# Performance work log

Hardware: AMD Instinct MI355X
Metric: run time of the kernel (lower is better)

The kernel has to match this reference:

```python
import jax, jax.numpy as jnp
import numpy as np

D = 512      # node_feature_size
LAT = 768    # latent_size
B = 16       # number of graphs
S = 256      # conditioning sequence length
H = 8        # attention heads


def _ln(x, g, b):
    m = x.mean(-1, keepdims=True)
    v = jnp.var(x, axis=-1, keepdims=True)
    return (x - m) / jnp.sqrt(v + 1e-5) * g + b


def setup_inputs() -> dict:
    key = jax.random.key(0)
    ks = jax.random.split(key, 10)
    lengths = np.array([512 + 32 * i for i in range(B)])  # ragged node counts
    N = int(lengths.sum())                                # 12032
    Lmax = int(lengths.max())                             # 992
    graph_batch = jnp.asarray(np.repeat(np.arange(B), lengths), dtype=jnp.int32)
    valid = np.array([S - 8 * i for i in range(B)])
    # torch key_padding_mask semantics: True = position is ignored (padding)
    conditioning_mask = jnp.asarray(np.arange(S)[None, :] >= valid[:, None])
    p = lambda k, sh: jax.random.normal(k, sh, jnp.float32) * 0.02
    return dict(
        graph_nodes=jax.random.normal(ks[0], (N, D), jnp.float32),
        graph_batch=graph_batch,
        conditioning_vector=jax.random.normal(ks[1], (B, S, LAT), jnp.float32),
        conditioning_mask=conditioning_mask,
        max_nodes=Lmax,
        num_heads=H,
        Wq=p(ks[2], (D, D)), bq=jnp.zeros(D, jnp.float32),
        Wk=p(ks[3], (LAT, D)), bk=jnp.zeros(D, jnp.float32),
        Wv=p(ks[4], (LAT, D)), bv=jnp.zeros(D, jnp.float32),
        in_w=p(ks[5], (3, D, D)), in_b=jnp.zeros((3, D), jnp.float32),
        Wo=p(ks[6], (D, D)), bo=jnp.zeros(D, jnp.float32),
        ln1_g=jnp.ones(D, jnp.float32), ln1_b=jnp.zeros(D, jnp.float32),
        W1=p(ks[7], (D, D)), b1=jnp.zeros(D, jnp.float32),
        ln2_g=jnp.ones(D, jnp.float32), ln2_b=jnp.zeros(D, jnp.float32),
    )


def reference(graph_nodes, graph_batch, conditioning_vector, conditioning_mask,
              max_nodes, num_heads, Wq, bq, Wk, bk, Wv, bv, in_w, in_b,
              Wo, bo, ln1_g, ln1_b, W1, b1, ln2_g, ln2_b):
    N, Dm = graph_nodes.shape
    Bn, Sk, _ = conditioning_vector.shape
    dh = Dm // num_heads
    # --- pad ragged node sets to dense [B, Lmax, D] (vectorized scatter) ---
    counts = jax.ops.segment_sum(jnp.ones(N, jnp.int32), graph_batch, num_segments=Bn)
    starts = jnp.concatenate([jnp.zeros(1, jnp.int32), jnp.cumsum(counts)[:-1].astype(jnp.int32)])
    pos = jnp.arange(N, dtype=jnp.int32) - starts[graph_batch]
    dense = jnp.zeros((Bn, max_nodes, Dm), graph_nodes.dtype).at[graph_batch, pos].set(graph_nodes)
    # --- projections ---
    q = dense @ Wq + bq
    k = conditioning_vector @ Wk + bk
    v = conditioning_vector @ Wv + bv
    # --- MultiheadAttention internal in-projections ---
    qh = (q @ in_w[0] + in_b[0]).reshape(Bn, max_nodes, num_heads, dh)
    kh = (k @ in_w[1] + in_b[1]).reshape(Bn, Sk, num_heads, dh)
    vh = (v @ in_w[2] + in_b[2]).reshape(Bn, Sk, num_heads, dh)
    scores = jnp.einsum('blhd,bshd->bhls', qh, kh) / jnp.sqrt(jnp.asarray(dh, qh.dtype))
    scores = jnp.where(conditioning_mask[:, None, None, :], -jnp.inf, scores)
    attn = jax.nn.softmax(scores, axis=-1)     # [B,H,L,S]
    av_attn = attn.mean(axis=1)                # head-averaged weights [B,L,S]
    ctx = jnp.einsum('bhls,bshd->blhd', attn, vh).reshape(Bn, max_nodes, Dm)
    attn_out = ctx @ Wo + bo
    # --- residual + LN + FFN + LN (dropout inactive / eval mode) ---
    x = _ln(attn_out + dense, ln1_g, ln1_b)
    x = jax.nn.leaky_relu(x @ W1 + b1) + x     # slope 0.01 matches nn.LeakyReLU
    x = _ln(x, ln2_g, ln2_b)
    # --- unpad back to ragged [N, D] (vectorized gather) ---
    node_out = x[graph_batch, pos]
    return node_out, av_attn
```

## Files before the change

### kernel.cpp

```cpp
#include <hip/hip_runtime.h>
#include <math.h>

#define D_   512
#define LAT_ 768
#define B_   16
#define S_   256
#define H_   8
#define DH_  64

typedef __bf16 bf16x8 __attribute__((ext_vector_type(8)));
typedef float f32x4 __attribute__((ext_vector_type(4)));

__device__ __forceinline__ unsigned short f2bf(float f) {
  unsigned u = __float_as_uint(f);
  unsigned r = (u + 0x7fffu + ((u >> 16) & 1u)) >> 16;
  return (unsigned short)r;
}

__global__ void prep_k(const void* __restrict__ mask, int* __restrict__ maskc,
                       const int* __restrict__ gb, int* __restrict__ starts, int n) {
  int i = blockIdx.x * blockDim.x + threadIdx.x;
  if (i < B_ * S_) {
    const unsigned char* pb = (const unsigned char*)mask;
    const int*   pi = (const int*)mask;
    const float* pf = (const float*)mask;
    unsigned int w = ((const unsigned int*)mask)[1023];
    int v;
    if (w == 0x01010101u)      v = pb[i];
    else if (w == 0x3f800000u) v = (pf[i] != 0.0f);
    else                       v = (pi[i] != 0);
    maskc[i] = v ? 1 : 0;
  }
  if (i < n) {
    if (i == 0 || gb[i] != gb[i - 1]) starts[gb[i]] = i;
  }
}

__global__ __launch_bounds__(256) void scatter_k(const float* __restrict__ nodes,
    const int* __restrict__ gb, const int* __restrict__ starts,
    float* __restrict__ dense, int Lmax) {
  int i = blockIdx.x;
  int b = gb[i], p = i - starts[b];
  const float* src = nodes + (size_t)i * D_;
  float* dst = dense + ((size_t)b * Lmax + p) * D_;
  dst[threadIdx.x]       = src[threadIdx.x];
  dst[threadIdx.x + 256] = src[threadIdx.x + 256];
}

__device__ __forceinline__ void pack_chunk(const float* __restrict__ W,
    unsigned short* __restrict__ out, int K, int ntoff, int idx) {
  int n = idx & 511, kc = idx >> 9;
  int kt = kc >> 2, kblk = kc & 3;
  int nt = n >> 7, nblk = (n >> 4) & 7, col = n & 15;
  int KT = K >> 5;
  size_t ob = ((size_t)((nt + ntoff) * KT + kt) * 4096) + nblk * 512 + kblk * 128 + col * 8;
  unsigned short v[8];
#pragma unroll
  for (int j = 0; j < 8; ++j) v[j] = f2bf(W[(size_t)(kc * 8 + j) * 512 + n]);
  int4 pk;
  pk.x = v[0] | (v[1] << 16); pk.y = v[2] | (v[3] << 16);
  pk.z = v[4] | (v[5] << 16); pk.w = v[6] | (v[7] << 16);
  *(int4*)&out[ob] = pk;
}

__global__ __launch_bounds__(256) void pack1_k(const float* __restrict__ in_w,
    const float* __restrict__ Wo, const float* __restrict__ W1,
    unsigned short* iw0, unsigned short* iw1, unsigned short* iw2,
    unsigned short* Wo_pk, unsigned short* W1_pk) {
  int bid = blockIdx.x, sel = bid >> 7, within = bid & 127;
  const float* W; unsigned short* out;
  switch (sel) {
    case 0: W = in_w;               out = iw0;   break;
    case 1: W = in_w + 512 * 512;   out = iw1;   break;
    case 2: W = in_w + 2 * 512 * 512; out = iw2; break;
    case 3: W = Wo;                 out = Wo_pk; break;
    default: W = W1;                out = W1_pk; break;
  }
  pack_chunk(W, out, 512, 0, within * 256 + threadIdx.x);
}

__global__ __launch_bounds__(256) void pack2_k(const float* __restrict__ Wqp,
    const float* __restrict__ Wkp, const float* __restrict__ Wvp,
    unsigned short* Wqp_pk, unsigned short* kv_pk) {
  int bid = blockIdx.x, tid = threadIdx.x;
  if (bid < 128)      pack_chunk(Wqp, Wqp_pk, 512, 0, bid * 256 + tid);
  else if (bid < 320) pack_chunk(Wkp, kv_pk, 768, 0, (bid - 128) * 256 + tid);
  else                pack_chunk(Wvp, kv_pk, 768, 4, (bid - 320) * 256 + tid);
}

__device__ __forceinline__ void mgemm64(const float* __restrict__ A,
    const unsigned short* __restrict__ Bpk, const float* __restrict__ bias,
    float* __restrict__ C, __bf16* __restrict__ Cb,
    int M, int N, int K, int xt, int yt,
    unsigned short* Al, unsigned short* Bl) {
  const int tid = threadIdx.x;
  const int lane = tid & 63, wid = tid >> 6;
  const int wr = wid >> 1, wc = wid & 1;
  const int row0 = yt * 64, col0 = xt * 128;
  const int KT = K >> 5;
  f32x4 acc[2][4];
#pragma unroll
  for (int m = 0; m < 2; ++m)
#pragma unroll
    for (int n = 0; n < 4; ++n) acc[m][n] = (f32x4){0.f, 0.f, 0.f, 0.f};
  const int kb0 = tid & 3, ar = tid >> 2;
  const unsigned short* bsrc = Bpk + (size_t)xt * KT * 4096;

  for (int kt = 0; kt < KT; ++kt) {
    {
      const unsigned short* g1 = bsrc + (size_t)kt * 4096 + wid * 512 + lane * 8;
      __builtin_amdgcn_global_load_lds(
          (const __attribute__((address_space(1))) void*)g1,
          (__attribute__((address_space(3))) void*)&Bl[wid * 512], 16, 0, 0);
      __builtin_amdgcn_global_load_lds(
          (const __attribute__((address_space(1))) void*)(g1 + 2048),
          (__attribute__((address_space(3))) void*)&Bl[2048 + wid * 512], 16, 0, 0);
    }
    {
      const float* ap = A + (size_t)(row0 + ar) * K + kt * 32 + kb0 * 8;
      float4 f0 = *(const float4*)ap;
      float4 f1 = *(const float4*)(ap + 4);
      int4 pk;
      pk.x = f2bf(f0.x) | (f2bf(f0.y) << 16);
      pk.y = f2bf(f0.z) | (f2bf(f0.w) << 16);
      pk.z = f2bf(f1.x) | (f2bf(f1.y) << 16);
      pk.w = f2bf(f1.z) | (f2bf(f1.w) << 16);
      *(int4*)&Al[(ar >> 4) * 512 + kb0 * 128 + (ar & 15) * 8] = pk;
    }
    __syncthreads();
    bf16x8 af[2], bfr[4];
#pragma unroll
    for (int m = 0; m < 2; ++m)
      af[m] = *(const bf16x8*)&Al[(wr * 2 + m) * 512 + lane * 8];
#pragma unroll
    for (int n = 0; n < 4; ++n)
      bfr[n] = *(const bf16x8*)&Bl[(wc * 4 + n) * 512 + lane * 8];
#pragma unroll
    for (int m = 0; m < 2; ++m)
#pragma unroll
      for (int n = 0; n < 4; ++n)
        acc[m][n] = __builtin_amdgcn_mfma_f32_16x16x32_bf16(af[m], bfr[n], acc[m][n], 0, 0, 0);
    __syncthreads();
  }
  const int cl = lane & 15, rg = lane >> 4;
  float bv[4];
#pragma unroll
  for (int n = 0; n < 4; ++n)
    bv[n] = bias ? bias[col0 + wc * 64 + n * 16 + cl] : 0.f;
#pragma unroll
  for (int m = 0; m < 2; ++m) {
    int r = row0 + wr * 32 + m * 16 + rg * 4;
#pragma unroll
    for (int n = 0; n < 4; ++n) {
      int c = col0 + wc * 64 + n * 16 + cl;
#pragma unroll
      for (int i = 0; i < 4; ++i) {
        float v = acc[m][n][i] + bv[n];
        if (Cb) Cb[(size_t)(r + i) * N + c] = (__bf16)v;
        else    C[(size_t)(r + i) * N + c] = v;
      }
    }
  }
}

__global__ __launch_bounds__(256) void gemm64_k(const float* __restrict__ A,
    const unsigned short* __restrict__ Bpk, const float* __restrict__ bias,
    float* __restrict__ C, int M, int N, int K) {
  __shared__ __align__(16) unsigned short Al[2048];
  __shared__ __align__(16) unsigned short Bl[4096];
  mgemm64(A, Bpk, bias, C, nullptr, M, N, K, blockIdx.x, blockIdx.y, Al, Bl);
}

__global__ __launch_bounds__(256) void fold_k(const float* __restrict__ Wq,
    const float* __restrict__ Wk, const float* __restrict__ Wv,
    const unsigned short* iw0, const unsigned short* iw1, const unsigned short* iw2,
    float* Wqp, float* Wkp, float* Wvp) {
  __shared__ __align__(16) unsigned short Al[2048];
  __shared__ __align__(16) unsigned short Bl[4096];
  int bid = blockIdx.x;
  if (bid < 32)       mgemm64(Wq, iw0, nullptr, Wqp, nullptr, 512, 512, 512, bid & 3, bid >> 2, Al, Bl);
  else if (bid < 80)  { int r = bid - 32; mgemm64(Wk, iw1, nullptr, Wkp, nullptr, 768, 512, 512, r & 3, r >> 2, Al, Bl); }
  else                { int r = bid - 80; mgemm64(Wv, iw2, nullptr, Wvp, nullptr, 768, 512, 512, r & 3, r >> 2, Al, Bl); }
}

__global__ __launch_bounds__(256) void proj_k(const float* __restrict__ dense,
    const float* __restrict__ cond, const unsigned short* Wqp_pk,
    const unsigned short* kv_pk, const float* __restrict__ bqp,
    const float* __restrict__ bkv, float* qh, __bf16* kvh, int BL) {
  __shared__ __align__(16) unsigned short Al[2048];
  __shared__ __align__(16) unsigned short Bl[4096];
  int bid = blockIdx.x;
  int nq = (BL >> 6) << 2;
  if (bid < nq)
    mgemm64(dense, Wqp_pk, bqp, qh, nullptr, BL, 512, 512, bid & 3, bid >> 2, Al, Bl);
  else {
    int r = bid - nq;
    mgemm64(cond, kv_pk, bkv, nullptr, kvh, B_ * S_, 1024, LAT_, r & 7, r >> 3, Al, Bl);
  }
}

__global__ void bias3_k(const float* __restrict__ bq, const float* __restrict__ bk,
    const float* __restrict__ bv, const float* __restrict__ in_w,
    const float* __restrict__ in_b, float* bqp, float* bkv) {
  int sel = blockIdx.x >> 1;
  int j = (blockIdx.x & 1) * 256 + threadIdx.x;
  const float* bin; const float* W; const float* badd; float* out;
  if (sel == 0)      { bin = bq; W = in_w;                 badd = in_b;          out = bqp; }
  else if (sel == 1) { bin = bk; W = in_w + 512 * 512;     badd = in_b + D_;     out = bkv; }
  else               { bin = bv; W = in_w + 2 * 512 * 512; badd = in_b + 2 * D_; out = bkv + 512; }
  float s = badd[j];
  for (int k = 0; k < D_; ++k) s += bin[k] * W[(size_t)k * D_ + j];
  out[j] = s;
}

__device__ __forceinline__ float rmax16(float v) {
  v = fmaxf(v, __shfl_xor(v, 1)); v = fmaxf(v, __shfl_xor(v, 2));
  v = fmaxf(v, __shfl_xor(v, 4)); v = fmaxf(v, __shfl_xor(v, 8));
  return v;
}
__device__ __forceinline__ float rsum16(float v) {
  v += __shfl_xor(v, 1); v += __shfl_xor(v, 2);
  v += __shfl_xor(v, 4); v += __shfl_xor(v, 8);
  return v;
}

__global__ __launch_bounds__(256) void attn_k(const float* __restrict__ qh,
    const __bf16* __restrict__ kvh, const int* __restrict__ maskc,
    float* __restrict__ ctx, float* __restrict__ avout, int Lmax) {
  const int bid = blockIdx.x;
  const int b = bid & 15;
  const int l0 = (bid >> 4) * 32;
  const int tid = threadIdx.x;
  const int lane = tid & 63, w = tid >> 6;
  const int lg = lane >> 4, l15 = lane & 15;
  __shared__ __align__(16) __bf16 v_lds[256][72];
  __shared__ __align__(16) __bf16 p_lds[32][264];
  __shared__ float maxred[4][32];
  __shared__ float sumred[4][32];
  __shared__ float mask_s[S_];
  mask_s[tid] = maskc[b * S_ + tid] ? -1.0e30f : 0.f;
  __syncthreads();
  float madd[4];
#pragma unroll
  for (int n = 0; n < 4; ++n) madd[n] = mask_s[w * 64 + n * 16 + l15];

  float av[2][4][4];
#pragma unroll
  for (int m = 0; m < 2; ++m)
#pragma unroll
    for (int n = 0; n < 4; ++n)
#pragma unroll
      for (int i = 0; i < 4; ++i) av[m][n][i] = 0.f;

  const size_t qrow0 = (size_t)b * Lmax + l0;
  const int srow = tid >> 2, scol = (tid & 3) * 16;

#pragma unroll 1
  for (int h = 0; h < H_; ++h) {
    __syncthreads();
#pragma unroll
    for (int pass = 0; pass < 4; ++pass) {
      int s = pass * 64 + srow;
      const __bf16* vp = kvh + (size_t)(b * S_ + s) * 1024 + 512 + h * DH_ + scol;
      *(bf16x8*)&v_lds[s][scol]     = *(const bf16x8*)vp;
      *(bf16x8*)&v_lds[s][scol + 8] = *(const bf16x8*)(vp + 8);
    }
    f32x4 qk[2][4];
#pragma unroll
    for (int m = 0; m < 2; ++m)
#pragma unroll
      for (int n = 0; n < 4; ++n) qk[m][n] = (f32x4){0.f, 0.f, 0.f, 0.f};
#pragma unroll
    for (int kt = 0; kt < 2; ++kt) {
      bf16x8 afr[2];
#pragma unroll
      for (int m = 0; m < 2; ++m) {
        const float* qp = qh + (qrow0 + m * 16 + l15) * D_ + h * DH_ + kt * 32 + lg * 8;
        float4 f0 = *(const float4*)qp, f1 = *(const float4*)(qp + 4);
        afr[m][0] = (__bf16)f0.x; afr[m][1] = (__bf16)f0.y;
        afr[m][2] = (__bf16)f0.z; afr[m][3] = (__bf16)f0.w;
        afr[m][4] = (__bf16)f1.x; afr[m][5] = (__bf16)f1.y;
        afr[m][6] = (__bf16)f1.z; afr[m][7] = (__bf16)f1.w;
      }
#pragma unroll
      for (int n = 0; n < 4; ++n) {
        const __bf16* kp = kvh + ((size_t)(b * S_) + w * 64 + n * 16 + l15) * 1024
                           + h * DH_ + kt * 32 + lg * 8;
        bf16x8 bfr = *(const bf16x8*)kp;
#pragma unroll
        for (int m = 0; m < 2; ++m)
          qk[m][n] = __builtin_amdgcn_mfma_f32_16x16x32_bf16(afr[m], bfr, qk[m][n], 0, 0, 0);
      }
    }
#pragma unroll
    for (int m = 0; m < 2; ++m)
#pragma unroll
      for (int n = 0; n < 4; ++n)
#pragma unroll
        for (int i = 0; i < 4; ++i)
          qk[m][n][i] = qk[m][n][i] * 0.125f + madd[n];
    float pm[2][4];
#pragma unroll
    for (int m = 0; m < 2; ++m)
#pragma unroll
      for (int i = 0; i < 4; ++i) {
        float v = fmaxf(fmaxf(qk[m][0][i], qk[m][1][i]), fmaxf(qk[m][2][i], qk[m][3][i]));
        pm[m][i] = rmax16(v);
      }
    if (l15 == 0) {
#pragma unroll
      for (int m = 0; m < 2; ++m)
#pragma unroll
        for (int i = 0; i < 4; ++i) maxred[w][m * 16 + lg * 4 + i] = pm[m][i];
    }
    __syncthreads();
    float gm[2][4], ps[2][4];
#pragma unroll
    for (int m = 0; m < 2; ++m)
#pragma unroll
      for (int i = 0; i < 4; ++i) {
        int row = m * 16 + lg * 4 + i;
        gm[m][i] = fmaxf(fmaxf(maxred[0][row], maxred[1][row]),
                         fmaxf(maxred[2][row], maxred[3][row]));
        ps[m][i] = 0.f;
      }
#pragma unroll
    for (int m = 0; m < 2; ++m)
#pragma unroll
      for (int n = 0; n < 4; ++n)
#pragma unroll
        for (int i = 0; i < 4; ++i) {
          float e = __expf(qk[m][n][i] - gm[m][i]);
          qk[m][n][i] = e;
          ps[m][i] += e;
        }
#pragma unroll
    for (int m = 0; m < 2; ++m)
#pragma unroll
      for (int i = 0; i < 4; ++i) pm[m][i] = rsum16(ps[m][i]);
    if (l15 == 0) {
#pragma unroll
      for (int m = 0; m < 2; ++m)
#pragma unroll
        for (int i = 0; i < 4; ++i) sumred[w][m * 16 + lg * 4 + i] = pm[m][i];
    }
    __syncthreads();
#pragma unroll
    for (int m = 0; m < 2; ++m)
#pragma unroll
      for (int i = 0; i < 4; ++i) {
        int row = m * 16 + lg * 4 + i;
        float inv = 1.f / (sumred[0][row] + sumred[1][row] + sumred[2][row] + sumred[3][row]);
#pragma unroll
        for (int n = 0; n < 4; ++n) {
          float p = qk[m][n][i] * inv;
          av[m][n][i] += p * 0.125f;
          p_lds[row][w * 64 + n * 16 + l15] = (__bf16)p;
        }
      }
    __syncthreads();
    f32x4 pv[2];
    pv[0] = (f32x4){0.f, 0.f, 0.f, 0.f};
    pv[1] = (f32x4){0.f, 0.f, 0.f, 0.f};
#pragma unroll
    for (int ks = 0; ks < 8; ++ks) {
      bf16x8 vb;
#pragma unroll
      for (int j = 0; j < 8; ++j) vb[j] = v_lds[ks * 32 + lg * 8 + j][w * 16 + l15];
#pragma unroll
      for (int m = 0; m < 2; ++m) {
        bf16x8 pa = *(const bf16x8*)&p_lds[m * 16 + l15][ks * 32 + lg * 8];
        pv[m] = __builtin_amdgcn_mfma_f32_16x16x32_bf16(pa, vb, pv[m], 0, 0, 0);
      }
    }
#pragma unroll
    for (int m = 0; m < 2; ++m)
#pragma unroll
      for (int i = 0; i < 4; ++i)
        ctx[(qrow0 + m * 16 + lg * 4 + i) * D_ + h * DH_ + w * 16 + l15] = pv[m][i];
  }
#pragma unroll
  for (int m = 0; m < 2; ++m)
#pragma unroll
    for (int i = 0; i < 4; ++i) {
      size_t arow = (qrow0 + m * 16 + lg * 4 + i) * S_;
#pragma unroll
      for (int n = 0; n < 4; ++n)
        avout[arow + w * 64 + n * 16 + l15] = av[m][n][i];
    }
}

__global__ __launch_bounds__(256) void ln_add_k(const float* __restrict__ a,
    const float* __restrict__ r, const float* __restrict__ g,
    const float* __restrict__ be, float* __restrict__ out) {
  size_t row = (size_t)blockIdx.x * D_;
  int tid = threadIdx.x;
  __shared__ float red[256];
  float v0 = a[row + tid]       + r[row + tid];
  float v1 = a[row + tid + 256] + r[row + tid + 256];
  red[tid] = v0 + v1;
  __syncthreads();
  for (int o = 128; o > 0; o >>= 1) { if (tid < o) red[tid] += red[tid + o]; __syncthreads(); }
  float mean = red[0] * (1.f / D_);
  __syncthreads();
  red[tid] = v0 * v0 + v1 * v1;
  __syncthreads();
  for (int o = 128; o > 0; o >>= 1) { if (tid < o) red[tid] += red[tid + o]; __syncthreads(); }
  float var = red[0] * (1.f / D_) - mean * mean;
  float rstd = rsqrtf(var + 1e-5f);
  out[row + tid]       = (v0 - mean) * rstd * g[tid]       + be[tid];
  out[row + tid + 256] = (v1 - mean) * rstd * g[tid + 256] + be[tid + 256];
}

__global__ __launch_bounds__(256) void final_k(const float* __restrict__ h1,
    const float* __restrict__ x1, const int* __restrict__ gb,
    const int* __restrict__ starts, const float* __restrict__ g,
    const float* __restrict__ be, float* __restrict__ out, int Lmax) {
  int i = blockIdx.x, tid = threadIdx.x;
  int b = gb[i], p = i - starts[b];
  size_t row = ((size_t)b * Lmax + p) * D_;
  __shared__ float red[256];
  float t0 = h1[row + tid];       t0 = (t0 >= 0.f) ? t0 : 0.01f * t0; t0 += x1[row + tid];
  float t1 = h1[row + tid + 256]; t1 = (t1 >= 0.f) ? t1 : 0.01f * t1; t1 += x1[row + tid + 256];
  red[tid] = t0 + t1;
  __syncthreads();
  for (int o = 128; o > 0; o >>= 1) { if (tid < o) red[tid] += red[tid + o]; __syncthreads(); }
  float mean = red[0] * (1.f / D_);
  __syncthreads();
  red[tid] = t0 * t0 + t1 * t1;
  __syncthreads();
  for (int o = 128; o > 0; o >>= 1) { if (tid < o) red[tid] += red[tid + o]; __syncthreads(); }
  float var = red[0] * (1.f / D_) - mean * mean;
  float rstd = rsqrtf(var + 1e-5f);
  out[(size_t)i * D_ + tid]       = (t0 - mean) * rstd * g[tid]       + be[tid];
  out[(size_t)i * D_ + tid + 256] = (t1 - mean) * rstd * g[tid + 256] + be[tid + 256];
}

extern "C" void kernel_launch(void* const* d_in, const int* in_sizes, int n_in,
                              void* d_out, int out_size, void* d_ws, size_t ws_size,
                              hipStream_t stream) {
  const float* nodes = (const float*)d_in[0];
  const int*   gb    = (const int*)d_in[1];
  const float* cond  = (const float*)d_in[2];
  const void*  maskp = d_in[3];
  const float* Wq   = (const float*)d_in[6];
  const float* bq   = (const float*)d_in[7];
  const float* Wk   = (const float*)d_in[8];
  const float* bk   = (const float*)d_in[9];
  const float* Wv   = (const float*)d_in[10];
  const float* bv   = (const float*)d_in[11];
  const float* in_w = (const float*)d_in[12];
  const float* in_b = (const float*)d_in[13];
  const float* Wo   = (const float*)d_in[14];
  const float* bo   = (const float*)d_in[15];
  const float* g1   = (const float*)d_in[16];
  const float* b1ln = (const float*)d_in[17];
  const float* W1   = (const float*)d_in[18];
  const float* b1f  = (const float*)d_in[19];
  const float* g2   = (const float*)d_in[20];
  const float* b2ln = (const float*)d_in[21];

  const int N    = in_sizes[0] / D_;
  const int Lmax = (out_size - N * D_) / (B_ * S_);
  const int BL   = B_ * Lmax;

  float* ws = (float*)d_ws;
  int* starts = (int*)(ws + 0);
  int* maskc  = (int*)(ws + 64);
  size_t o = 8192;
  float* dense = ws + o; o += (size_t)BL * D_;
  float* qh    = ws + o; o += (size_t)BL * D_;
  float* ctx   = qh;
  __bf16* kvh  = (__bf16*)(ws + o); o += (size_t)B_ * S_ * 1024 / 2;
  float* tmp   = ws + o; o += (size_t)BL * D_;
  float* x1    = ws + o; o += (size_t)BL * D_;
  float* h1    = dense;
  float* Wqp = ws + o; o += (size_t)D_ * D_;
  float* Wkp = ws + o; o += (size_t)LAT_ * D_;
  float* Wvp = ws + o; o += (size_t)LAT_ * D_;
  float* bqp = ws + o; o += D_;
  float* bkv = ws + o; o += 1024;
  unsigned short* iw0_pk = (unsigned short*)(ws + o); o += (size_t)D_ * D_ / 2;
  unsigned short* iw1_pk = (unsigned short*)(ws + o); o += (size_t)D_ * D_ / 2;
  unsigned short* iw2_pk = (unsigned short*)(ws + o); o += (size_t)D_ * D_ / 2;
  unsigned short* Wqp_pk = (unsigned short*)(ws + o); o += (size_t)D_ * D_ / 2;
  unsigned short* kv_pk  = (unsigned short*)(ws + o); o += (size_t)LAT_ * 1024 / 2;
  unsigned short* Wo_pk  = (unsigned short*)(ws + o); o += (size_t)D_ * D_ / 2;
  unsigned short* W1_pk  = (unsigned short*)(ws + o); o += (size_t)D_ * D_ / 2;

  (void)hipMemsetAsync(d_ws, 0, (8192 + (size_t)BL * D_) * sizeof(float), stream);

  prep_k<<<(N + 255) / 256, 256, 0, stream>>>(maskp, maskc, gb, starts, N);
  scatter_k<<<N, 256, 0, stream>>>(nodes, gb, starts, dense, Lmax);

  pack1_k<<<640, 256, 0, stream>>>(in_w, Wo, W1, iw0_pk, iw1_pk, iw2_pk, Wo_pk, W1_pk);
  fold_k<<<128, 256, 0, stream>>>(Wq, Wk, Wv, iw0_pk, iw1_pk, iw2_pk, Wqp, Wkp, Wvp);
  pack2_k<<<512, 256, 0, stream>>>(Wqp, Wkp, Wvp, Wqp_pk, kv_pk);
  bias3_k<<<6, 256, 0, stream>>>(bq, bk, bv, in_w, in_b, bqp, bkv);

  proj_k<<<(BL >> 6) * 4 + 512, 256, 0, stream>>>(dense, cond, Wqp_pk, kv_pk,
      bqp, bkv, qh, kvh, BL);

  attn_k<<<(Lmax / 32) * B_, 256, 0, stream>>>(qh, kvh, maskc, ctx,
      (float*)d_out + (size_t)N * D_, Lmax);

  gemm64_k<<<dim3(4, BL / 64), 256, 0, stream>>>(ctx, Wo_pk, bo, tmp, BL, D_, D_);
  ln_add_k<<<BL, 256, 0, stream>>>(tmp, dense, g1, b1ln, x1);

  gemm64_k<<<dim3(4, BL / 64), 256, 0, stream>>>(x1, W1_pk, b1f, h1, BL, D_, D_);
  final_k<<<N, 256, 0, stream>>>(h1, x1, gb, starts, g2, b2ln, (float*)d_out, Lmax);
}
```

Before: 250.5 us.

## Split attention block across eight waves instead of four

The attention kernel now launches 512 threads per block. Each of the eight waves handles 32 key columns for QK/softmax and one 16x16 output tile for PV, instead of 64 columns and two tiles. The padding of the V and P shared-memory arrays changes, and the mask is read directly from global memory instead of being staged in LDS. This aims to raise parallelism and latency hiding per block, at the cost of more cross-wave reduction traffic, and the new padding may change bank-conflict behaviour.

```diff
diff --git a/kernel.cpp b/kernel.cpp
--- a/kernel.cpp
+++ b/kernel.cpp
@@ -224,7 +224,7 @@
   return v;
 }
 
-__global__ __launch_bounds__(256) void attn_k(const float* __restrict__ qh,
+__global__ __launch_bounds__(512) void attn_k(const float* __restrict__ qh,
     const __bf16* __restrict__ kvh, const int* __restrict__ maskc,
     float* __restrict__ ctx, float* __restrict__ avout, int Lmax) {
   const int bid = blockIdx.x;
@@ -233,43 +233,43 @@
   const int tid = threadIdx.x;
   const int lane = tid & 63, w = tid >> 6;
   const int lg = lane >> 4, l15 = lane & 15;
-  __shared__ __align__(16) __bf16 v_lds[256][72];
-  __shared__ __align__(16) __bf16 p_lds[32][264];
-  __shared__ float maxred[4][32];
-  __shared__ float sumred[4][32];
-  __shared__ float mask_s[S_];
-  mask_s[tid] = maskc[b * S_ + tid] ? -1.0e30f : 0.f;
-  __syncthreads();
-  float madd[4];
-#pragma unroll
-  for (int n = 0; n < 4; ++n) madd[n] = mask_s[w * 64 + n * 16 + l15];
-
-  float av[2][4][4];
+  __shared__ __align__(16) __bf16 v_lds[256][68];
+  __shared__ __align__(16) __bf16 p_lds[32][260];
+  __shared__ float maxred[8][32];
+  __shared__ float sumred[8][32];
+
+  float madd[2];
+#pragma unroll
+  for (int n = 0; n < 2; ++n)
+    madd[n] = maskc[b * S_ + w * 32 + n * 16 + l15] ? -1.0e30f : 0.f;
+
+  float av[2][2][4];
 #pragma unroll
   for (int m = 0; m < 2; ++m)
 #pragma unroll
-    for (int n = 0; n < 4; ++n)
+    for (int n = 0; n < 2; ++n)
 #pragma unroll
       for (int i = 0; i < 4; ++i) av[m][n][i] = 0.f;
 
   const size_t qrow0 = (size_t)b * Lmax + l0;
-  const int srow = tid >> 2, scol = (tid & 3) * 16;
+  const int vrow = tid >> 1, vcol0 = (tid & 1) * 32;
+  const int m2 = w & 1, dt = w >> 1;
 
 #pragma unroll 1
   for (int h = 0; h < H_; ++h) {
     __syncthreads();
-#pragma unroll
-    for (int pass = 0; pass < 4; ++pass) {
-      int s = pass * 64 + srow;
-      const __bf16* vp = kvh + (size_t)(b * S_ + s) * 1024 + 512 + h * DH_ + scol;
-      *(bf16x8*)&v_lds[s][scol]     = *(const bf16x8*)vp;
-      *(bf16x8*)&v_lds[s][scol + 8] = *(const bf16x8*)(vp + 8);
-    }
-    f32x4 qk[2][4];
-#pragma unroll
-    for (int m = 0; m < 2; ++m)
-#pragma unroll
-      for (int n = 0; n < 4; ++n) qk[m][n] = (f32x4){0.f, 0.f, 0.f, 0.f};
+    {
+      const __bf16* vp = kvh + (size_t)(b * S_ + vrow) * 1024 + 512 + h * DH_ + vcol0;
+      *(bf16x8*)&v_lds[vrow][vcol0]      = *(const bf16x8*)vp;
+      *(bf16x8*)&v_lds[vrow][vcol0 + 8]  = *(const bf16x8*)(vp + 8);
+      *(bf16x8*)&v_lds[vrow][vcol0 + 16] = *(const bf16x8*)(vp + 16);
+      *(bf16x8*)&v_lds[vrow][vcol0 + 24] = *(const bf16x8*)(vp + 24);
+    }
+    f32x4 qk[2][2];
+#pragma unroll
+    for (int m = 0; m < 2; ++m)
+#pragma unroll
+      for (int n = 0; n < 2; ++n) qk[m][n] = (f32x4){0.f, 0.f, 0.f, 0.f};
 #pragma unroll
     for (int kt = 0; kt < 2; ++kt) {
       bf16x8 afr[2];
@@ -283,8 +283,8 @@
         afr[m][6] = (__bf16)f1.z; afr[m][7] = (__bf16)f1.w;
       }
 #pragma unroll
-      for (int n = 0; n < 4; ++n) {
-        const __bf16* kp = kvh + ((size_t)(b * S_) + w * 64 + n * 16 + l15) * 1024
+      for (int n = 0; n < 2; ++n) {
+        const __bf16* kp = kvh + ((size_t)(b * S_) + w * 32 + n * 16 + l15) * 1024
                            + h * DH_ + kt * 32 + lg * 8;
         bf16x8 bfr = *(const bf16x8*)kp;
 #pragma unroll
@@ -295,7 +295,7 @@
 #pragma unroll
     for (int m = 0; m < 2; ++m)
 #pragma unroll
-      for (int n = 0; n < 4; ++n)
+      for (int n = 0; n < 2; ++n)
 #pragma unroll
         for (int i = 0; i < 4; ++i)
           qk[m][n][i] = qk[m][n][i] * 0.125f + madd[n];
@@ -303,10 +303,8 @@
 #pragma unroll
     for (int m = 0; m < 2; ++m)
 #pragma unroll
-      for (int i = 0; i < 4; ++i) {
-        float v = fmaxf(fmaxf(qk[m][0][i], qk[m][1][i]), fmaxf(qk[m][2][i], qk[m][3][i]));
-        pm[m][i] = rmax16(v);
-      }
+      for (int i = 0; i < 4; ++i)
+        pm[m][i] = rmax16(fmaxf(qk[m][0][i], qk[m][1][i]));
     if (l15 == 0) {
 #pragma unroll
       for (int m = 0; m < 2; ++m)
@@ -320,14 +318,17 @@
 #pragma unroll
       for (int i = 0; i < 4; ++i) {
         int row = m * 16 + lg * 4 + i;
-        gm[m][i] = fmaxf(fmaxf(maxred[0][row], maxred[1][row]),
+        float g0 = fmaxf(fmaxf(maxred[0][row], maxred[1][row]),
                          fmaxf(maxred[2][row], maxred[3][row]));
+        float g1 = fmaxf(fmaxf(maxred[4][row], maxred[5][row]),
+                         fmaxf(maxred[6][row], maxred[7][row]));
+        gm[m][i] = fmaxf(g0, g1);
         ps[m][i] = 0.f;
       }
 #pragma unroll
     for (int m = 0; m < 2; ++m)
 #pragma unroll
-      for (int n = 0; n < 4; ++n)
+      for (int n = 0; n < 2; ++n)
 #pragma unroll
         for (int i = 0; i < 4; ++i) {
           float e = __expf(qk[m][n][i] - gm[m][i]);
@@ -350,34 +351,29 @@
 #pragma unroll
       for (int i = 0; i < 4; ++i) {
         int row = m * 16 + lg * 4 + i;
-        float inv = 1.f / (sumred[0][row] + sumred[1][row] + sumred[2][row] + sumred[3][row]);
-#pragma unroll
-        for (int n = 0; n < 4; ++n) {
+        float denom = (sumred[0][row] + sumred[1][row]) + (sumred[2][row] + sumred[3][row])
+                    + (sumred[4][row] + sumred[5][row]) + (sumred[6][row] + sumred[7][row]);
+        float inv = 1.f / denom;
+#pragma unroll
+        for (int n = 0; n < 2; ++n) {
           float p = qk[m][n][i] * inv;
           av[m][n][i] += p * 0.125f;
-          p_lds[row][w * 64 + n * 16 + l15] = (__bf16)p;
+          p_lds[row][w * 32 + n * 16 + l15] = (__bf16)p;
         }
       }
     __syncthreads();
-    f32x4 pv[2];
-    pv[0] = (f32x4){0.f, 0.f, 0.f, 0.f};
-    pv[1] = (f32x4){0.f, 0.f, 0.f, 0.f};
+    f32x4 pv = (f32x4){0.f, 0.f, 0.f, 0.f};
 #pragma unroll
     for (int ks = 0; ks < 8; ++ks) {
       bf16x8 vb;
 #pragma unroll
-      for (int j = 0; j < 8; ++j) vb[j] = v_lds[ks * 32 + lg * 8 + j][w * 16 + l15];
-#pragma unroll
-      for (int m = 0; m < 2; ++m) {
-        bf16x8 pa = *(const bf16x8*)&p_lds[m * 16 + l15][ks * 32 + lg * 8];
-        pv[m] = __builtin_amdgcn_mfma_f32_16x16x32_bf16(pa, vb, pv[m], 0, 0, 0);
-      }
-    }
-#pragma unroll
-    for (int m = 0; m < 2; ++m)
-#pragma unroll
-      for (int i = 0; i < 4; ++i)
-        ctx[(qrow0 + m * 16 + lg * 4 + i) * D_ + h * DH_ + w * 16 + l15] = pv[m][i];
+      for (int j = 0; j < 8; ++j) vb[j] = v_lds[ks * 32 + lg * 8 + j][dt * 16 + l15];
+      bf16x8 pa = *(const bf16x8*)&p_lds[m2 * 16 + l15][ks * 32 + lg * 8];
+      pv = __builtin_amdgcn_mfma_f32_16x16x32_bf16(pa, vb, pv, 0, 0, 0);
+    }
+#pragma unroll
+    for (int i = 0; i < 4; ++i)
+      ctx[(qrow0 + m2 * 16 + lg * 4 + i) * D_ + h * DH_ + dt * 16 + l15] = pv[i];
   }
 #pragma unroll
   for (int m = 0; m < 2; ++m)
@@ -385,8 +381,8 @@
     for (int i = 0; i < 4; ++i) {
       size_t arow = (qrow0 + m * 16 + lg * 4 + i) * S_;
 #pragma unroll
-      for (int n = 0; n < 4; ++n)
-        avout[arow + w * 64 + n * 16 + l15] = av[m][n][i];
+      for (int n = 0; n < 2; ++n)
+        avout[arow + w * 32 + n * 16 + l15] = av[m][n][i];
     }
 }
 
@@ -501,7 +497,7 @@
   proj_k<<<(BL >> 6) * 4 + 512, 256, 0, stream>>>(dense, cond, Wqp_pk, kv_pk,
       bqp, bkv, qh, kvh, BL);
 
-  attn_k<<<(Lmax / 32) * B_, 256, 0, stream>>>(qh, kvh, maskc, ctx,
+  attn_k<<<(Lmax / 32) * B_, 512, 0, stream>>>(qh, kvh, maskc, ctx,
       (float*)d_out + (size_t)N * D_, Lmax);
 
   gemm64_k<<<dim3(4, BL / 64), 256, 0, stream>>>(ctx, Wo_pk, bo, tmp, BL, D_, D_);
```

Measured after the change: 273.2 us. 1.09x slower.
